# Optimization experiments

Hardware: AMD Instinct MI355X
Metric: run time of the kernel (lower is better)

The kernel has to match this reference:

```python
import jax, jax.numpy as jnp
import numpy as np

B, D, T = 16384, 1024, 128  # batch, embed_dim, num_degradation_types
V, L = 4, 3                 # variants per sample, degradations per variant


def setup_inputs() -> dict:
    key = jax.random.key(0)
    k1, k2, k3, k4 = jax.random.split(key, 4)
    clean_embeddings = jax.random.normal(k1, (B, D), dtype=jnp.float32)
    W = jax.random.normal(k2, (T, D), dtype=jnp.float32) * (1.0 / np.sqrt(D))
    b = jnp.zeros((T,), dtype=jnp.float32)
    deg_indices = jax.random.randint(k3, (B, V, L), 0, T, dtype=jnp.int32)
    deg_mask = jax.random.randint(k4, (B, V, L), 0, 2, dtype=jnp.int32)
    return {"clean_embeddings": clean_embeddings, "W": W, "b": b,
            "deg_indices": deg_indices, "deg_mask": deg_mask}


def reference(clean_embeddings, W, b, deg_indices, deg_mask):
    # Linear + softmax: [B, T]
    logits = jnp.einsum("bd,td->bt", clean_embeddings, W) + b
    probs = jax.nn.softmax(logits, axis=-1)
    # Gather probs at each (batch, label) pair: [B, V*L] -> [B, V, L]
    flat_idx = deg_indices.reshape(B, V * L)
    gathered = jnp.take_along_axis(probs, flat_idx, axis=1).reshape(B, V, L)
    # Masked sum over all labels of a sample, divided by max(num_variants, 1)=V
    per_sample = (gathered * deg_mask.astype(probs.dtype)).sum(axis=(1, 2)) / V
    return per_sample.sum() / B
```

## Files before the change

### kernel.cpp

```cpp
#include <hip/hip_runtime.h>

#define B_SIZE 16384
#define D_DIM  1024
#define T_DIM  128
#define VLn    12
#define BM     32
#define NCHUNK 16
#define GRID   (B_SIZE / BM)
#define ASTR   66
#define ABUF   8448
#define SL_STRIDE 132

typedef _Float16 half8  __attribute__((ext_vector_type(8)));
typedef __fp16   fp16x2 __attribute__((ext_vector_type(2)));
typedef float    f32x4  __attribute__((ext_vector_type(4)));

union Pack16 { fp16x2 h[4]; uint4 u; half8 v; };
union Frag   { uint4 u; half8 h; };

__device__ __forceinline__ uint4 pack8u(float4 v0, float4 v1) {
    Pack16 un;
    un.h[0] = __builtin_amdgcn_cvt_pkrtz(v0.x, v0.y);
    un.h[1] = __builtin_amdgcn_cvt_pkrtz(v0.z, v0.w);
    un.h[2] = __builtin_amdgcn_cvt_pkrtz(v1.x, v1.y);
    un.h[3] = __builtin_amdgcn_cvt_pkrtz(v1.z, v1.w);
    return un.u;
}
__device__ __forceinline__ half8 pack8h(float4 v0, float4 v1) {
    Pack16 un;
    un.h[0] = __builtin_amdgcn_cvt_pkrtz(v0.x, v0.y);
    un.h[1] = __builtin_amdgcn_cvt_pkrtz(v0.z, v0.w);
    un.h[2] = __builtin_amdgcn_cvt_pkrtz(v1.x, v1.y);
    un.h[3] = __builtin_amdgcn_cvt_pkrtz(v1.z, v1.w);
    return un.v;
}

__global__ __launch_bounds__(256)
void conv_w(const float* __restrict__ W, uint4* __restrict__ Wf) {
    const int j    = blockIdx.x * 256 + threadIdx.x;
    const int kc   = j >> 10;
    const int r    = j & 1023;
    const int g    = r >> 6;
    const int lane = r & 63;
    const int n = (g & 7) * 16 + (lane & 15);
    const int k = kc * 64 + (g >> 3) * 32 + ((lane >> 4) << 3);
    const float* src = W + (size_t)n * D_DIM + k;
    Wf[j] = pack8u(*(const float4*)src, *(const float4*)(src + 4));
}

__global__ __launch_bounds__(256, 2)
void qloss_kernel(const float* __restrict__ emb,
                  const uint4* __restrict__ Wf,
                  const float* __restrict__ bias,
                  const int*   __restrict__ didx,
                  const int*   __restrict__ dmsk,
                  float*       __restrict__ out)
{
    __shared__ __align__(16) unsigned char smem[2 * ABUF + 16];
    float* sL   = (float*)smem;
    float* sRed = (float*)(smem + 2 * ABUF);

    const int t    = threadIdx.x;
    const int w    = t >> 6;
    const int lane = t & 63;
    const int m15  = lane & 15;
    const int quad = lane >> 4;
    const int r0   = blockIdx.x * BM;

    const int arow = t >> 3;
    const int acol = (t & 7) * 4;
    const float* aG = emb + (size_t)(r0 + arow) * D_DIM + acol;
    float* aL = (float*)smem + arow * ASTR + acol;

    const int frBase = m15 * ASTR + quad * 8;

    const uint4* bP = Wf + (size_t)(2 * w) * 64 + lane;

    f32x4 acc[2][2];
#pragma unroll
    for (int mt = 0; mt < 2; ++mt)
#pragma unroll
        for (int ct = 0; ct < 2; ++ct) acc[mt][ct] = (f32x4){0.f, 0.f, 0.f, 0.f};

    Frag bc[4], bn1[4], bn2[4];
    float4 a1v0, a1v1, a2v0, a2v1;

    {
        const float4 v0 = *(const float4*)(aG);
        const float4 v1 = *(const float4*)(aG + 32);
        a1v0 = *(const float4*)(aG + 64);
        a1v1 = *(const float4*)(aG + 96);
#pragma unroll
        for (int ks = 0; ks < 2; ++ks)
#pragma unroll
            for (int j = 0; j < 2; ++j) {
                bc[ks * 2 + j].u  = bP[(size_t)(ks * 8 + j) * 64];
                bn1[ks * 2 + j].u = bP[(size_t)1 * 1024 + (ks * 8 + j) * 64];
            }
        *(float4*)(aL)      = v0;
        *(float4*)(aL + 32) = v1;
    }
    __syncthreads();

#pragma unroll
    for (int kc = 0; kc < NCHUNK; ++kc) {
        float* bufC = (float*)(smem + (kc & 1) * ABUF);
        float* bufN = (float*)(smem + ((kc & 1) ^ 1) * ABUF);

        if (kc + 2 < NCHUNK) {
            a2v0 = *(const float4*)(aG + (kc + 2) * 64);
            a2v1 = *(const float4*)(aG + (kc + 2) * 64 + 32);
#pragma unroll
            for (int ks = 0; ks < 2; ++ks)
#pragma unroll
                for (int j = 0; j < 2; ++j)
                    bn2[ks * 2 + j].u = bP[(size_t)(kc + 2) * 1024 + (ks * 8 + j) * 64];
        }

#pragma unroll
        for (int ks = 0; ks < 2; ++ks) {
#pragma unroll
            for (int mt = 0; mt < 2; ++mt) {
                const float* fp = bufC + mt * 16 * ASTR + frBase + ks * 32;
                const float4 lo = *(const float4*)(fp);
                const float4 hi = *(const float4*)(fp + 4);
                const half8 a = pack8h(lo, hi);
                acc[mt][0] = __builtin_amdgcn_mfma_f32_16x16x32_f16(a, bc[ks * 2 + 0].h, acc[mt][0], 0, 0, 0);
                acc[mt][1] = __builtin_amdgcn_mfma_f32_16x16x32_f16(a, bc[ks * 2 + 1].h, acc[mt][1], 0, 0, 0);
            }
        }

        if (kc + 1 < NCHUNK) {
            float* wp = bufN + arow * ASTR + acol;
            *(float4*)(wp)      = a1v0;
            *(float4*)(wp + 32) = a1v1;
        }
        __syncthreads();

        a1v0 = a2v0; a1v1 = a2v1;
#pragma unroll
        for (int q = 0; q < 4; ++q) { bc[q] = bn1[q]; bn1[q] = bn2[q]; }
    }

    const int CT0 = w * 2;
    const float b0v = bias[CT0 * 16 + m15];
    const float b1v = bias[(CT0 + 1) * 16 + m15];
#pragma unroll
    for (int mt = 0; mt < 2; ++mt)
#pragma unroll
        for (int i = 0; i < 4; ++i) {
            const int row = mt * 16 + quad * 4 + i;
            sL[row * SL_STRIDE + CT0 * 16 + m15]       = acc[mt][0][i] + b0v;
            sL[row * SL_STRIDE + (CT0 + 1) * 16 + m15] = acc[mt][1][i] + b1v;
        }
    __syncthreads();

    {
        const int row = t >> 3, s = t & 7;
        float* base = &sL[row * SL_STRIDE + s * 16];
        float v[16];
#pragma unroll
        for (int j = 0; j < 4; ++j) *(float4*)&v[j * 4] = *(const float4*)(base + j * 4);
        float m = -1e30f;
#pragma unroll
        for (int j = 0; j < 16; ++j) m = fmaxf(m, v[j]);
#pragma unroll
        for (int off = 1; off < 8; off <<= 1) m = fmaxf(m, __shfl_xor(m, off));
        float ssum = 0.f;
#pragma unroll
        for (int j = 0; j < 16; ++j) { v[j] = __expf(v[j] - m); ssum += v[j]; }
#pragma unroll
        for (int off = 1; off < 8; off <<= 1) ssum += __shfl_xor(ssum, off);
        const float inv = 1.0f / ssum;
#pragma unroll
        for (int j = 0; j < 16; ++j) v[j] *= inv;
#pragma unroll
        for (int j = 0; j < 4; ++j) *(float4*)(base + j * 4) = *(const float4*)&v[j * 4];
    }
    __syncthreads();

    float p = 0.f;
#pragma unroll
    for (int i = t; i < BM * VLn; i += 256) {
        const int gi  = r0 * VLn + i;
        const int row = i / VLn;
        const int idx = didx[gi];
        const int mk  = dmsk[gi];
        p += mk ? sL[row * SL_STRIDE + idx] : 0.f;
    }
#pragma unroll
    for (int off = 1; off < 64; off <<= 1) p += __shfl_xor(p, off);
    if (lane == 0) sRed[w] = p;
    __syncthreads();
    if (t == 0)
        atomicAdd(out, (sRed[0] + sRed[1] + sRed[2] + sRed[3]) * (1.0f / 65536.0f));
}

extern "C" void kernel_launch(void* const* d_in, const int* in_sizes, int n_in,
                              void* d_out, int out_size, void* d_ws, size_t ws_size,
                              hipStream_t stream) {
    const float* emb  = (const float*)d_in[0];
    const float* W    = (const float*)d_in[1];
    const float* bias = (const float*)d_in[2];
    const int*   didx = (const int*)d_in[3];
    const int*   dmsk = (const int*)d_in[4];
    float* out = (float*)d_out;

    uint4* Wf = (uint4*)d_ws;

    hipMemsetAsync(out, 0, sizeof(float), stream);
    conv_w<<<64, 256, 0, stream>>>(W, Wf);
    qloss_kernel<<<GRID, 256, 0, stream>>>(emb, Wf, bias, didx, dmsk, out);
}
```

Before: 129.4 us.

## Use direct global-to-LDS loads with 16-row tiles and 256-wide K chunks

Halves the rows per block to 16, which doubles the grid to 1024 blocks, and raises the K chunk to 256 so there are 4 chunks instead of 16. Embedding tiles now go straight from global memory into LDS through global_load_lds instead of being staged in registers. The change aims to cut register pressure and the number of barrier iterations, and to improve latency hiding through more blocks in flight. In exchange each block reads the W fragments for only 16 rows, so W reuse per block drops, and the LDS buffers are larger.

```diff
diff --git a/kernel.cpp b/kernel.cpp
--- a/kernel.cpp
+++ b/kernel.cpp
@@ -4,12 +4,14 @@
 #define D_DIM  1024
 #define T_DIM  128
 #define VLn    12
-#define BM     32
-#define NCHUNK 16
+#define BM     16
+#define BK     256
+#define NCHUNK 4
 #define GRID   (B_SIZE / BM)
-#define ASTR   66
-#define ABUF   8448
-#define SL_STRIDE 132
+#define AROWF  258
+#define AROWB  1032
+#define ABUFB  (BM * AROWB)
+#define SLSTR  132
 
 typedef _Float16 half8  __attribute__((ext_vector_type(8)));
 typedef __fp16   fp16x2 __attribute__((ext_vector_type(2)));
@@ -26,13 +28,23 @@
     un.h[3] = __builtin_amdgcn_cvt_pkrtz(v1.z, v1.w);
     return un.u;
 }
-__device__ __forceinline__ half8 pack8h(float4 v0, float4 v1) {
+__device__ __forceinline__ half8 pack8f(const float* fp) {
+    const float2 a = ((const float2*)fp)[0];
+    const float2 b = ((const float2*)fp)[1];
+    const float2 c = ((const float2*)fp)[2];
+    const float2 d = ((const float2*)fp)[3];
     Pack16 un;
-    un.h[0] = __builtin_amdgcn_cvt_pkrtz(v0.x, v0.y);
-    un.h[1] = __builtin_amdgcn_cvt_pkrtz(v0.z, v0.w);
-    un.h[2] = __builtin_amdgcn_cvt_pkrtz(v1.x, v1.y);
-    un.h[3] = __builtin_amdgcn_cvt_pkrtz(v1.z, v1.w);
+    un.h[0] = __builtin_amdgcn_cvt_pkrtz(a.x, a.y);
+    un.h[1] = __builtin_amdgcn_cvt_pkrtz(b.x, b.y);
+    un.h[2] = __builtin_amdgcn_cvt_pkrtz(c.x, c.y);
+    un.h[3] = __builtin_amdgcn_cvt_pkrtz(d.x, d.y);
     return un.v;
+}
+
+__device__ __forceinline__ void dma16(const float* g, void* l) {
+    __builtin_amdgcn_global_load_lds(
+        (__attribute__((address_space(1))) void*)g,
+        (__attribute__((address_space(3))) void*)l, 16, 0, 0);
 }
 
 __global__ __launch_bounds__(256)
@@ -56,9 +68,9 @@
                   const int*   __restrict__ dmsk,
                   float*       __restrict__ out)
 {
-    __shared__ __align__(16) unsigned char smem[2 * ABUF + 16];
+    __shared__ __align__(16) unsigned char smem[2 * ABUFB + 16];
     float* sL   = (float*)smem;
-    float* sRed = (float*)(smem + 2 * ABUF);
+    float* sRed = (float*)(smem + 2 * ABUFB);
 
     const int t    = threadIdx.x;
     const int w    = t >> 6;
@@ -67,126 +79,103 @@
     const int quad = lane >> 4;
     const int r0   = blockIdx.x * BM;
 
-    const int arow = t >> 3;
-    const int acol = (t & 7) * 4;
-    const float* aG = emb + (size_t)(r0 + arow) * D_DIM + acol;
-    float* aL = (float*)smem + arow * ASTR + acol;
-
-    const int frBase = m15 * ASTR + quad * 8;
-
-    const uint4* bP = Wf + (size_t)(2 * w) * 64 + lane;
-
-    f32x4 acc[2][2];
-#pragma unroll
-    for (int mt = 0; mt < 2; ++mt)
-#pragma unroll
-        for (int ct = 0; ct < 2; ++ct) acc[mt][ct] = (f32x4){0.f, 0.f, 0.f, 0.f};
-
-    Frag bc[4], bn1[4], bn2[4];
-    float4 a1v0, a1v1, a2v0, a2v1;
-
-    {
-        const float4 v0 = *(const float4*)(aG);
-        const float4 v1 = *(const float4*)(aG + 32);
-        a1v0 = *(const float4*)(aG + 64);
-        a1v1 = *(const float4*)(aG + 96);
-#pragma unroll
-        for (int ks = 0; ks < 2; ++ks)
-#pragma unroll
-            for (int j = 0; j < 2; ++j) {
-                bc[ks * 2 + j].u  = bP[(size_t)(ks * 8 + j) * 64];
-                bn1[ks * 2 + j].u = bP[(size_t)1 * 1024 + (ks * 8 + j) * 64];
-            }
-        *(float4*)(aL)      = v0;
-        *(float4*)(aL + 32) = v1;
+    const float* aG0 = emb + (size_t)(r0 + 4 * w) * D_DIM + lane * 4;
+
+    const uint4* bP = Wf + lane;
+    const int CT0 = 2 * w;
+
+    f32x4 acc[2];
+    acc[0] = (f32x4){0.f, 0.f, 0.f, 0.f};
+    acc[1] = (f32x4){0.f, 0.f, 0.f, 0.f};
+
+    Frag bc[16], bn[16];
+
+#pragma unroll
+    for (int r = 0; r < 4; ++r)
+        dma16(aG0 + (size_t)r * D_DIM, smem + (4 * w + r) * AROWB);
+#pragma unroll
+    for (int ks = 0; ks < 8; ++ks) {
+        const int s = ks;
+#pragma unroll
+        for (int j = 0; j < 2; ++j)
+            bc[ks * 2 + j].u = bP[(size_t)(s >> 1) * 1024 + ((s & 1) * 8 + CT0 + j) * 64];
     }
     __syncthreads();
 
 #pragma unroll
     for (int kc = 0; kc < NCHUNK; ++kc) {
-        float* bufC = (float*)(smem + (kc & 1) * ABUF);
-        float* bufN = (float*)(smem + ((kc & 1) ^ 1) * ABUF);
-
-        if (kc + 2 < NCHUNK) {
-            a2v0 = *(const float4*)(aG + (kc + 2) * 64);
-            a2v1 = *(const float4*)(aG + (kc + 2) * 64 + 32);
-#pragma unroll
-            for (int ks = 0; ks < 2; ++ks)
+        const unsigned char* bufC = smem + (kc & 1) * ABUFB;
+        unsigned char*       bufN = (unsigned char*)smem + ((kc & 1) ^ 1) * ABUFB;
+
+        if (kc + 1 < NCHUNK) {
+#pragma unroll
+            for (int r = 0; r < 4; ++r)
+                dma16(aG0 + (size_t)r * D_DIM + (kc + 1) * BK,
+                      bufN + (4 * w + r) * AROWB);
+#pragma unroll
+            for (int ks = 0; ks < 8; ++ks) {
+                const int s = (kc + 1) * 8 + ks;
 #pragma unroll
                 for (int j = 0; j < 2; ++j)
-                    bn2[ks * 2 + j].u = bP[(size_t)(kc + 2) * 1024 + (ks * 8 + j) * 64];
-        }
-
-#pragma unroll
-        for (int ks = 0; ks < 2; ++ks) {
-#pragma unroll
-            for (int mt = 0; mt < 2; ++mt) {
-                const float* fp = bufC + mt * 16 * ASTR + frBase + ks * 32;
-                const float4 lo = *(const float4*)(fp);
-                const float4 hi = *(const float4*)(fp + 4);
-                const half8 a = pack8h(lo, hi);
-                acc[mt][0] = __builtin_amdgcn_mfma_f32_16x16x32_f16(a, bc[ks * 2 + 0].h, acc[mt][0], 0, 0, 0);
-                acc[mt][1] = __builtin_amdgcn_mfma_f32_16x16x32_f16(a, bc[ks * 2 + 1].h, acc[mt][1], 0, 0, 0);
+                    bn[ks * 2 + j].u =
+                        bP[(size_t)(s >> 1) * 1024 + ((s & 1) * 8 + CT0 + j) * 64];
             }
         }
 
-        if (kc + 1 < NCHUNK) {
-            float* wp = bufN + arow * ASTR + acol;
-            *(float4*)(wp)      = a1v0;
-            *(float4*)(wp + 32) = a1v1;
+#pragma unroll
+        for (int ks = 0; ks < 8; ++ks) {
+            const float* fp = (const float*)bufC + m15 * AROWF + ks * 32 + quad * 8;
+            const half8 a = pack8f(fp);
+            acc[0] = __builtin_amdgcn_mfma_f32_16x16x32_f16(a, bc[ks * 2 + 0].h, acc[0], 0, 0, 0);
+            acc[1] = __builtin_amdgcn_mfma_f32_16x16x32_f16(a, bc[ks * 2 + 1].h, acc[1], 0, 0, 0);
         }
         __syncthreads();
 
-        a1v0 = a2v0; a1v1 = a2v1;
-#pragma unroll
-        for (int q = 0; q < 4; ++q) { bc[q] = bn1[q]; bn1[q] = bn2[q]; }
-    }
-
-    const int CT0 = w * 2;
+#pragma unroll
+        for (int q = 0; q < 16; ++q) bc[q] = bn[q];
+    }
+
     const float b0v = bias[CT0 * 16 + m15];
     const float b1v = bias[(CT0 + 1) * 16 + m15];
 #pragma unroll
-    for (int mt = 0; mt < 2; ++mt)
-#pragma unroll
-        for (int i = 0; i < 4; ++i) {
-            const int row = mt * 16 + quad * 4 + i;
-            sL[row * SL_STRIDE + CT0 * 16 + m15]       = acc[mt][0][i] + b0v;
-            sL[row * SL_STRIDE + (CT0 + 1) * 16 + m15] = acc[mt][1][i] + b1v;
-        }
+    for (int i = 0; i < 4; ++i) {
+        const int row = quad * 4 + i;
+        sL[row * SLSTR + CT0 * 16 + m15]       = acc[0][i] + b0v;
+        sL[row * SLSTR + (CT0 + 1) * 16 + m15] = acc[1][i] + b1v;
+    }
     __syncthreads();
 
     {
-        const int row = t >> 3, s = t & 7;
-        float* base = &sL[row * SL_STRIDE + s * 16];
-        float v[16];
-#pragma unroll
-        for (int j = 0; j < 4; ++j) *(float4*)&v[j * 4] = *(const float4*)(base + j * 4);
+        const int row = t >> 4, s = t & 15;
+        float* base = &sL[row * SLSTR + s * 8];
+        float v[8];
+        *(float4*)&v[0] = *(const float4*)(base);
+        *(float4*)&v[4] = *(const float4*)(base + 4);
         float m = -1e30f;
 #pragma unroll
-        for (int j = 0; j < 16; ++j) m = fmaxf(m, v[j]);
-#pragma unroll
-        for (int off = 1; off < 8; off <<= 1) m = fmaxf(m, __shfl_xor(m, off));
+        for (int j = 0; j < 8; ++j) m = fmaxf(m, v[j]);
+#pragma unroll
+        for (int off = 1; off < 16; off <<= 1) m = fmaxf(m, __shfl_xor(m, off));
         float ssum = 0.f;
 #pragma unroll
-        for (int j = 0; j < 16; ++j) { v[j] = __expf(v[j] - m); ssum += v[j]; }
-#pragma unroll
-        for (int off = 1; off < 8; off <<= 1) ssum += __shfl_xor(ssum, off);
+        for (int j = 0; j < 8; ++j) { v[j] = __expf(v[j] - m); ssum += v[j]; }
+#pragma unroll
+        for (int off = 1; off < 16; off <<= 1) ssum += __shfl_xor(ssum, off);
         const float inv = 1.0f / ssum;
 #pragma unroll
-        for (int j = 0; j < 16; ++j) v[j] *= inv;
-#pragma unroll
-        for (int j = 0; j < 4; ++j) *(float4*)(base + j * 4) = *(const float4*)&v[j * 4];
+        for (int j = 0; j < 8; ++j) v[j] *= inv;
+        *(float4*)(base)     = *(const float4*)&v[0];
+        *(float4*)(base + 4) = *(const float4*)&v[4];
     }
     __syncthreads();
 
     float p = 0.f;
-#pragma unroll
-    for (int i = t; i < BM * VLn; i += 256) {
-        const int gi  = r0 * VLn + i;
-        const int row = i / VLn;
+    if (t < BM * VLn) {
+        const int gi  = r0 * VLn + t;
+        const int row = t / VLn;
         const int idx = didx[gi];
         const int mk  = dmsk[gi];
-        p += mk ? sL[row * SL_STRIDE + idx] : 0.f;
+        p = mk ? sL[row * SLSTR + idx] : 0.f;
     }
 #pragma unroll
     for (int off = 1; off < 64; off <<= 1) p += __shfl_xor(p, off);
```

New measurement: 114.3 us. 11.7% less time.
